# Optimization experiments

Hardware: AMD Instinct MI355X
Metric: run time of the kernel (lower is better)

Reference implementation:

```python
import jax, jax.numpy as jnp
import numpy as np

B, N, DIM = 2, 8192, 3
K = 16            # num_neighbours (dilation=1)
R = 2048          # num_representitives
CIN, CL, COUT = 64, 16, 128
K2 = K * K


def _bn(x, g, b):
    # BatchNorm in eval mode with running_mean=0, running_var=1 -> affine
    return x * g + b


def setup_inputs() -> dict:
    key = jax.random.key(0)
    ks = jax.random.split(key, 24)
    r = lambda i, shape, s=1.0: jax.random.normal(ks[i], shape, jnp.float32) * s
    return {
        "points": r(0, (B, N, DIM)),
        "features": r(1, (B, N, CIN)),
        "lift_w": r(2, (CL, DIM), 0.3), "lift_b": r(3, (CL,), 0.1),
        "bn_lift_g": 1.0 + r(4, (CL,), 0.1), "bn_lift_b": r(5, (CL,), 0.1),
        "t1_w": r(6, (K2, DIM * K), 0.1), "t1_b": r(7, (K2,), 0.1),
        "bn1_g": 1.0 + r(8, (K2,), 0.1), "bn1_b": r(9, (K2,), 0.1),
        "t2_w": r(10, (K2, K2), 0.05), "t2_b": r(11, (K2,), 0.1),
        "bn2_g": 1.0 + r(12, (K2,), 0.1), "bn2_b": r(13, (K2,), 0.1),
        "t3_w": r(14, (K2, K2), 0.05), "t3_b": r(15, (K2,), 0.1),
        "bn3_g": 1.0 + r(16, (K2,), 0.1), "bn3_b": r(17, (K2,), 0.1),
        "conv_w": r(18, (COUT, CIN + CL, K), 0.05), "conv_b": r(19, (COUT,), 0.1),
        "rep_idx": jax.random.permutation(ks[20], N)[:R],
    }


def reference(points, features, lift_w, lift_b, bn_lift_g, bn_lift_b,
              t1_w, t1_b, bn1_g, bn1_b, t2_w, t2_b, bn2_g, bn2_b,
              t3_w, t3_b, bn3_g, bn3_b, conv_w, conv_b, rep_idx):
    b, n, _ = points.shape
    # ---- KNN (squared distance is order-equivalent to torch.cdist) ----
    sq = jnp.sum(points * points, -1)                                   # (b,n)
    d2 = sq[:, :, None] + sq[:, None, :] - 2.0 * jnp.einsum('bnd,bmd->bnm', points, points)
    _, idx = jax.lax.top_k(-d2, K + 1)                                  # (b,n,K+1)
    nn_idx = idx[:, :, 1:]                                              # drop self
    # ---- representative sampling + neighbor gather ----
    rep_pos = points[:, rep_idx]                                        # (b,R,3)
    nb_idx = nn_idx[:, rep_idx]                                         # (b,R,K)
    gather = jax.vmap(lambda arr, i: arr[i])
    nbr_pos = gather(points, nb_idx)                                    # (b,R,K,3)
    nbr_feat = gather(features, nb_idx)                                 # (b,R,K,CIN)
    # ---- X_conv ----
    p = (nbr_pos - rep_pos[:, :, None, :]).reshape(b * R, K, DIM)       # centered
    lifted = jax.nn.relu(_bn(p @ lift_w.T + lift_b, bn_lift_g, bn_lift_b))  # (bR,K,CL)
    feat = jnp.concatenate([lifted, nbr_feat.reshape(b * R, K, CIN)], -1)   # (bR,K,CL+CIN)
    pf = p.reshape(b * R, K * DIM)
    h = jax.nn.relu(_bn(pf @ t1_w.T + t1_b, bn1_g, bn1_b))
    h = jax.nn.relu(_bn(h @ t2_w.T + t2_b, bn2_g, bn2_b))
    T = _bn(h @ t3_w.T + t3_b, bn3_g, bn3_b).reshape(b * R, K, K)       # learned transform
    Tf = jnp.einsum('bij,bjc->bic', T, feat)                            # bmm, (bR,K,C)
    # Conv1d(C, COUT, kernel=K) over length K -> single output position
    out = jnp.einsum('bkc,ock->bo', Tf, conv_w) + conv_b                # (bR,COUT)
    return rep_pos, out.reshape(b, R, COUT)
```

## Files before the change

kernel.cpp:

```cpp
#include <hip/hip_runtime.h>
#include <float.h>

#define Bn 2
#define Nn 8192
#define Rr 2048
#define Kk 16
#define CIN 64
#define CL 16
#define COUT 128
#define K2c 256
#define GT (Bn*Rr)
#define FD (CL+CIN)
#define KC (Kk*FD)
#define MG 8
#define SPLITK 4
#define CCAP 128

__global__ __launch_bounds__(256) void prep_kernel(
    const float* __restrict__ t1_w, const float* __restrict__ t2_w,
    const float* __restrict__ t3_w, const float* __restrict__ conv_w,
    const float* __restrict__ points,
    float* __restrict__ t1t, float* __restrict__ t2t,
    float* __restrict__ t3t, float* __restrict__ wp,
    float4* __restrict__ pts4)
{
  int i = blockIdx.x * 256 + threadIdx.x;
  if (i < K2c*48) { int j = i / 48, k = i - j*48; t1t[k*K2c + j] = t1_w[i]; }
  if (i < K2c*K2c) { int j = i >> 8, k = i & 255; t2t[k*K2c + j] = t2_w[i]; t3t[k*K2c + j] = t3_w[i]; }
  if (i < COUT*KC) {
    int o = i / KC, ck = i - o*KC;
    int c = ck >> 4, k = ck & 15;
    wp[(k*FD + c)*COUT + o] = conv_w[i];
  }
  if (i < Bn*Nn) {
    float x = points[i*3+0], y = points[i*3+1], z = points[i*3+2];
    float sq = __fadd_rn(__fadd_rn(__fmul_rn(x,x), __fmul_rn(y,y)), __fmul_rn(z,z));
    pts4[i] = make_float4(x, y, z, sq);
  }
}

__global__ __launch_bounds__(512, 4) void knn_kernel(
    const float4* __restrict__ pts4, const int* __restrict__ rep_idx,
    int* __restrict__ nb_idx, float* __restrict__ p_out,
    float* __restrict__ rep_pos_out)
{
  __shared__ float cbuf[8][512];
  __shared__ unsigned long long coll[8][CCAP];
  __shared__ float Lst[8][64];
  __shared__ float4 qS[8];
  __shared__ float  tauS[8];
  __shared__ int    ccnt[8];

  int t    = threadIdx.x;
  int lane = t & 63;
  int w    = t >> 6;
  int g0   = blockIdx.x * 8;
  int b    = g0 >> 11;
  const float4* pb4 = pts4 + (size_t)b*Nn;

  if (t < 8) {
    int g = g0 + t;
    int r = g & 2047;
    qS[t] = pb4[rep_idx[r]];
    ccnt[t] = 0;
  }
  __syncthreads();

  float qx[8], qy[8], qz[8], qw[8];
  #pragma unroll
  for (int q = 0; q < 8; q++) {
    float4 Q = qS[q];
    qx[q] = __uint_as_float(__builtin_amdgcn_readfirstlane(__float_as_uint(Q.x)));
    qy[q] = __uint_as_float(__builtin_amdgcn_readfirstlane(__float_as_uint(Q.y)));
    qz[q] = __uint_as_float(__builtin_amdgcn_readfirstlane(__float_as_uint(Q.z)));
    qw[q] = __uint_as_float(__builtin_amdgcn_readfirstlane(__float_as_uint(Q.w)));
  }

  float m[8];
  #pragma unroll
  for (int q = 0; q < 8; q++) m[q] = FLT_MAX;
  for (int i0 = 0; i0 < 16; i0 += 4) {
    float4 P0 = pb4[t + 512*(i0+0)];
    float4 P1 = pb4[t + 512*(i0+1)];
    float4 P2 = pb4[t + 512*(i0+2)];
    float4 P3 = pb4[t + 512*(i0+3)];
    #pragma unroll
    for (int q = 0; q < 8; q++) {
      float d0 = __fsub_rn(__fadd_rn(qw[q], P0.w), __fmul_rn(2.0f,
                 __fmaf_rn(qz[q], P0.z, __fmaf_rn(qy[q], P0.y, __fmul_rn(qx[q], P0.x)))));
      float d1 = __fsub_rn(__fadd_rn(qw[q], P1.w), __fmul_rn(2.0f,
                 __fmaf_rn(qz[q], P1.z, __fmaf_rn(qy[q], P1.y, __fmul_rn(qx[q], P1.x)))));
      float d2 = __fsub_rn(__fadd_rn(qw[q], P2.w), __fmul_rn(2.0f,
                 __fmaf_rn(qz[q], P2.z, __fmaf_rn(qy[q], P2.y, __fmul_rn(qx[q], P2.x)))));
      float d3 = __fsub_rn(__fadd_rn(qw[q], P3.w), __fmul_rn(2.0f,
                 __fmaf_rn(qz[q], P3.z, __fmaf_rn(qy[q], P3.y, __fmul_rn(qx[q], P3.x)))));
      m[q] = fminf(fminf(fminf(m[q], d0), fminf(d1, d2)), d3);
    }
  }

  #pragma unroll
  for (int q = 0; q < 8; q++) cbuf[q][t] = m[q];
  __syncthreads();

  {
    float C0 = FLT_MAX, C1 = FLT_MAX, C2 = FLT_MAX;
    #pragma unroll
    for (int j = 0; j < 8; j++) {
      float v = cbuf[w][lane + 64*j];
      float n2 = __builtin_amdgcn_fmed3f(C1, C2, v);
      float n1 = __builtin_amdgcn_fmed3f(C0, C1, v);
      float n0 = fminf(C0, v);
      C0 = n0; C1 = n1; C2 = n2;
    }
    Lst[w][lane] = C2;
  }
  __syncthreads();
  {
    float L = Lst[w][lane];
    int rk = 0;
    #pragma unroll 8
    for (int i = 0; i < 64; i++) {
      float Li = Lst[w][i];
      rk += (Li < L || (Li == L && i < lane)) ? 1 : 0;
    }
    if (rk == 5) tauS[w] = L;
  }
  __syncthreads();

  float tau[8];
  #pragma unroll
  for (int q = 0; q < 8; q++)
    tau[q] = __uint_as_float(__builtin_amdgcn_readfirstlane(__float_as_uint(tauS[q])));

  for (int i0 = 0; i0 < 16; i0 += 4) {
    float4 Pb[4];
    Pb[0] = pb4[t + 512*(i0+0)];
    Pb[1] = pb4[t + 512*(i0+1)];
    Pb[2] = pb4[t + 512*(i0+2)];
    Pb[3] = pb4[t + 512*(i0+3)];
    #pragma unroll
    for (int u = 0; u < 4; u++) {
      float4 P = Pb[u];
      int idx = t + 512*(i0+u);
      #pragma unroll
      for (int q = 0; q < 8; q++) {
        float dot = __fmaf_rn(qz[q], P.z, __fmaf_rn(qy[q], P.y, __fmul_rn(qx[q], P.x)));
        float d2  = __fsub_rn(__fadd_rn(qw[q], P.w), __fmul_rn(2.0f, dot));
        if (d2 <= tau[q]) {
          int pos = atomicAdd(&ccnt[q], 1);
          if (pos < CCAP) {
            unsigned f = __float_as_uint(d2);
            unsigned mono = f ^ ((unsigned)((int)f >> 31) | 0x80000000u);
            coll[q][pos] = ((unsigned long long)mono << 32) | (unsigned)idx;
          }
        }
      }
    }
  }
  __syncthreads();

  int cnt = __builtin_amdgcn_readfirstlane(ccnt[w]);
  if (cnt > CCAP) cnt = CCAP;
  unsigned long long k1 = (lane < cnt)      ? coll[w][lane]      : ~0ull;
  unsigned long long k2 = (lane + 64 < cnt) ? coll[w][lane + 64] : ~0ull;
  int r1 = 0, r2 = 0;
  for (int i = 0; i < cnt; i++) {
    unsigned long long ki = coll[w][i];
    r1 += (ki < k1) ? 1 : 0;
    r2 += (ki < k2) ? 1 : 0;
  }

  int g = g0 + w;
  float4 Q = qS[w];
  if (lane < cnt && r1 >= 1 && r1 <= 16) {
    int om = (int)(k1 & 0xFFFFFFFFull);
    nb_idx[g*Kk + r1 - 1] = om;
    float4 Pm = pb4[om];
    p_out[(g*Kk + r1 - 1)*3 + 0] = __fsub_rn(Pm.x, Q.x);
    p_out[(g*Kk + r1 - 1)*3 + 1] = __fsub_rn(Pm.y, Q.y);
    p_out[(g*Kk + r1 - 1)*3 + 2] = __fsub_rn(Pm.z, Q.z);
  }
  if (lane + 64 < cnt && r2 >= 1 && r2 <= 16) {
    int om = (int)(k2 & 0xFFFFFFFFull);
    nb_idx[g*Kk + r2 - 1] = om;
    float4 Pm = pb4[om];
    p_out[(g*Kk + r2 - 1)*3 + 0] = __fsub_rn(Pm.x, Q.x);
    p_out[(g*Kk + r2 - 1)*3 + 1] = __fsub_rn(Pm.y, Q.y);
    p_out[(g*Kk + r2 - 1)*3 + 2] = __fsub_rn(Pm.z, Q.z);
  }
  if (lane < 3) rep_pos_out[g*3 + lane] = (lane == 0 ? Q.x : (lane == 1 ? Q.y : Q.z));
}

__device__ __forceinline__ void fma_g(float4& a, float hv, const float4& wv) {
  a.x = fmaf(hv, wv.x, a.x);
  a.y = fmaf(hv, wv.y, a.y);
  a.z = fmaf(hv, wv.z, a.z);
  a.w = fmaf(hv, wv.w, a.w);
}

__global__ __launch_bounds__(256) void mlp_kernel(
    const float* __restrict__ p,
    const float* __restrict__ t1t, const float* __restrict__ t1_b,
    const float* __restrict__ g1v, const float* __restrict__ b1v,
    const float* __restrict__ t2t, const float* __restrict__ t2_b,
    const float* __restrict__ g2v, const float* __restrict__ b2v,
    const float* __restrict__ t3t, const float* __restrict__ t3_b,
    const float* __restrict__ g3v, const float* __restrict__ b3v,
    float* __restrict__ T_out)
{
  __shared__ float pf[48][MG];
  __shared__ float hA[K2c][MG];
  __shared__ float red[4*32*66];
  int t = threadIdx.x;
  int w = t >> 6, l = t & 63;
  int g0 = blockIdx.x * MG;
  for (int e = t; e < MG*48; e += 256) {
    int g = e / 48, k = e - g*48;
    pf[k][g] = p[(size_t)(g0+g)*48 + k];
  }
  __syncthreads();

  float4 acc[MG];

#define LDW(WSRC, K) (*(const float4*)&WSRC[(size_t)(K)*K2c + 4*l])

#define KSTAGE(WSRC, KDIM, HBUF, WB, KK, KNEXT)                        \
  {                                                                    \
    float4 wc = WB;                                                    \
    if ((KNEXT) < KDIM) WB = LDW(WSRC, KNEXT);                         \
    float4 ha = *(const float4*)&HBUF[KK][0];                          \
    float4 hb = *(const float4*)&HBUF[KK][4];                          \
    fma_g(acc[0], ha.x, wc); fma_g(acc[1], ha.y, wc);                  \
    fma_g(acc[2], ha.z, wc); fma_g(acc[3], ha.w, wc);                  \
    fma_g(acc[4], hb.x, wc); fma_g(acc[5], hb.y, wc);                  \
    fma_g(acc[6], hb.z, wc); fma_g(acc[7], hb.w, wc);                  \
  }

#define KLOOP(WSRC, KDIM, HBUF)                                        \
  {                                                                    \
    _Pragma("unroll")                                                  \
    for (int q = 0; q < MG; q++) acc[q] = make_float4(0.f,0.f,0.f,0.f);\
    float4 wb0 = LDW(WSRC, w);                                         \
    float4 wb1 = (w + 4  < KDIM) ? LDW(WSRC, w + 4)  : wb0;            \
    float4 wb2 = (w + 8  < KDIM) ? LDW(WSRC, w + 8)  : wb0;            \
    float4 wb3 = (w + 12 < KDIM) ? LDW(WSRC, w + 12) : wb0;            \
    for (int k = w; k < KDIM; k += 16) {                               \
      KSTAGE(WSRC, KDIM, HBUF, wb0, k,      k + 16)                    \
      if (k + 4 < KDIM)  KSTAGE(WSRC, KDIM, HBUF, wb1, k + 4,  k + 20) \
      if (k + 8 < KDIM)  KSTAGE(WSRC, KDIM, HBUF, wb2, k + 8,  k + 24) \
      if (k + 12 < KDIM) KSTAGE(WSRC, KDIM, HBUF, wb3, k + 12, k + 28) \
    }                                                                  \
  }

#define WRITE_RED()                                                    \
  {                                                                    \
    _Pragma("unroll")                                                  \
    for (int q = 0; q < MG; q++) {                                     \
      red[(w*32 + 0*8 + q)*66 + l] = acc[q].x;                         \
      red[(w*32 + 1*8 + q)*66 + l] = acc[q].y;                         \
      red[(w*32 + 2*8 + q)*66 + l] = acc[q].z;                         \
      red[(w*32 + 3*8 + q)*66 + l] = acc[q].w;                         \
    }                                                                  \
  }

#define REDUCE(S)                                                      \
  float S[MG];                                                         \
  {                                                                    \
    int lr = t >> 2, cc = t & 3;                                       \
    _Pragma("unroll")                                                  \
    for (int q = 0; q < MG; q++) S[q] = 0.f;                           \
    _Pragma("unroll")                                                  \
    for (int ww = 0; ww < 4; ww++) {                                   \
      _Pragma("unroll")                                                \
      for (int q = 0; q < MG; q++)                                     \
        S[q] += red[(ww*32 + cc*8 + q)*66 + lr];                       \
    }                                                                  \
  }

  KLOOP(t1t, 48, pf)
  WRITE_RED()
  __syncthreads();
  {
    REDUCE(s)
    float bb = t1_b[t], gg = g1v[t], oo = b1v[t];
    float4 v0, v1;
    v0.x = fmaxf(fmaf(s[0] + bb, gg, oo), 0.f);
    v0.y = fmaxf(fmaf(s[1] + bb, gg, oo), 0.f);
    v0.z = fmaxf(fmaf(s[2] + bb, gg, oo), 0.f);
    v0.w = fmaxf(fmaf(s[3] + bb, gg, oo), 0.f);
    v1.x = fmaxf(fmaf(s[4] + bb, gg, oo), 0.f);
    v1.y = fmaxf(fmaf(s[5] + bb, gg, oo), 0.f);
    v1.z = fmaxf(fmaf(s[6] + bb, gg, oo), 0.f);
    v1.w = fmaxf(fmaf(s[7] + bb, gg, oo), 0.f);
    *(float4*)&hA[t][0] = v0;
    *(float4*)&hA[t][4] = v1;
  }
  __syncthreads();

  KLOOP(t2t, K2c, hA)
  WRITE_RED()
  __syncthreads();
  {
    REDUCE(s)
    float bb = t2_b[t], gg = g2v[t], oo = b2v[t];
    float4 v0, v1;
    v0.x = fmaxf(fmaf(s[0] + bb, gg, oo), 0.f);
    v0.y = fmaxf(fmaf(s[1] + bb, gg, oo), 0.f);
    v0.z = fmaxf(fmaf(s[2] + bb, gg, oo), 0.f);
    v0.w = fmaxf(fmaf(s[3] + bb, gg, oo), 0.f);
    v1.x = fmaxf(fmaf(s[4] + bb, gg, oo), 0.f);
    v1.y = fmaxf(fmaf(s[5] + bb, gg, oo), 0.f);
    v1.z = fmaxf(fmaf(s[6] + bb, gg, oo), 0.f);
    v1.w = fmaxf(fmaf(s[7] + bb, gg, oo), 0.f);
    *(float4*)&hA[t][0] = v0;
    *(float4*)&hA[t][4] = v1;
  }
  __syncthreads();

  KLOOP(t3t, K2c, hA)
  WRITE_RED()
  __syncthreads();
  {
    REDUCE(s)
    float bb = t3_b[t], gg = g3v[t], oo = b3v[t];
    #pragma unroll
    for (int q = 0; q < MG; q++)
      T_out[(size_t)(g0+q)*K2c + t] = fmaf(s[q] + bb, gg, oo);
  }
#undef KLOOP
#undef KSTAGE
#undef LDW
#undef WRITE_RED
#undef REDUCE
}

__global__ __launch_bounds__(256) void tf_kernel(
    const float* __restrict__ T_in, const float* __restrict__ features,
    const float* __restrict__ p, const int* __restrict__ nb_idx,
    const float* __restrict__ lift_w, const float* __restrict__ lift_b,
    const float* __restrict__ bng, const float* __restrict__ bnb,
    float* __restrict__ Tf)
{
  __shared__ float T_s[4*K2c];
  __shared__ float f_s[4*KC];
  __shared__ float ps[4*48];
  __shared__ int   idxs[64];
  __shared__ float lw[48], lb2[16], lg[16], lo[16];
  int t = threadIdx.x;
  int g0 = blockIdx.x * 4;
  int b = g0 / Rr;
  for (int e = t; e < 4*K2c; e += 256) T_s[e] = T_in[(size_t)g0*K2c + e];
  if (t >= 32 && t < 224) {
    int e = t - 32;
    ps[e] = p[(size_t)g0*48 + e];
  }
  if (t < 64) idxs[t] = nb_idx[g0*16 + t];
  if (t >= 64 && t < 112)  lw[t-64]   = lift_w[t-64];
  if (t >= 112 && t < 128) lb2[t-112] = lift_b[t-112];
  if (t >= 224 && t < 240) lg[t-224]  = bng[t-224];
  if (t >= 240)            lo[t-240]  = bnb[t-240];
  __syncthreads();

  {
    int wv = t >> 6, ln = t & 63;
    for (int row = wv; row < 64; row += 4) {
      int gg = row >> 4, k = row & 15;
      f_s[gg*KC + k*FD + CL + ln] = features[((size_t)b*Nn + idxs[row])*CIN + ln];
    }
  }
  for (int e = t; e < 1024; e += 256) {
    int gg = e >> 8, rem = e & 255, k = rem >> 4, c = rem & 15;
    float acc = ps[gg*48 + k*3 + 0]*lw[c*3+0] + ps[gg*48 + k*3 + 1]*lw[c*3+1]
              + ps[gg*48 + k*3 + 2]*lw[c*3+2] + lb2[c];
    acc = acc*lg[c] + lo[c];
    f_s[gg*KC + k*FD + c] = fmaxf(acc, 0.f);
  }
  __syncthreads();

  int gg = t >> 6;
  int cl = t & 63;
  for (int ci = cl; ci < FD; ci += 64) {
    float fcol[16];
    #pragma unroll
    for (int j = 0; j < 16; j++) fcol[j] = f_s[gg*KC + j*FD + ci];
    #pragma unroll
    for (int k = 0; k < 16; k++) {
      float acc = 0.f;
      #pragma unroll
      for (int j = 0; j < 16; j++) acc = fmaf(T_s[gg*K2c + k*16 + j], fcol[j], acc);
      Tf[(size_t)(g0+gg)*KC + k*FD + ci] = acc;
    }
  }
}

__global__ __launch_bounds__(256) void gemm_kernel(
    const float* __restrict__ A,
    const float* __restrict__ Bm,
    float* __restrict__ part)
{
  __shared__ float As[16*36];
  __shared__ float Bs[16*COUT];
  int t = threadIdx.x;
  int m0 = blockIdx.x * 32;
  int ky = blockIdx.y;
  int kbase0 = ky * (KC/SPLITK);
  float acc[4][4];
  #pragma unroll
  for (int i = 0; i < 4; i++)
    #pragma unroll
    for (int j = 0; j < 4; j++) acc[i][j] = 0.f;
  int tn = t & 31, tm = t >> 5;

  for (int kt = 0; kt < KC/SPLITK; kt += 16) {
    int kb = kbase0 + kt;
    {
      int kcol = t & 15, row = t >> 4;
      As[kcol*36 + row]      = A[(size_t)(m0+row)*KC + kb + kcol];
      As[kcol*36 + row + 16] = A[(size_t)(m0+row+16)*KC + kb + kcol];
    }
    {
      int o = t & 127, kk2 = t >> 7;
      #pragma unroll
      for (int p4 = 0; p4 < 8; p4++) {
        int kk = kk2 + p4*2;
        Bs[kk*COUT + o] = Bm[(size_t)(kb+kk)*COUT + o];
      }
    }
    __syncthreads();
    #pragma unroll
    for (int kk = 0; kk < 16; kk++) {
      float4 a4 = *(const float4*)&As[kk*36 + tm*4];
      float4 b4 = *(const float4*)&Bs[kk*COUT + tn*4];
      float av[4] = {a4.x, a4.y, a4.z, a4.w};
      float bv[4] = {b4.x, b4.y, b4.z, b4.w};
      #pragma unroll
      for (int i = 0; i < 4; i++)
        #pragma unroll
        for (int j = 0; j < 4; j++) acc[i][j] = fmaf(av[i], bv[j], acc[i][j]);
    }
    __syncthreads();
  }
  #pragma unroll
  for (int i = 0; i < 4; i++) {
    float4 v = make_float4(acc[i][0], acc[i][1], acc[i][2], acc[i][3]);
    *(float4*)&part[((size_t)ky*GT + m0 + tm*4 + i)*COUT + tn*4] = v;
  }
}

__global__ __launch_bounds__(256) void reduce_kernel(
    const float* __restrict__ part, const float* __restrict__ conv_b,
    float* __restrict__ outp)
{
  int i = blockIdx.x*256 + threadIdx.x;
  float4 s = ((const float4*)conv_b)[i & 31];
  #pragma unroll
  for (int w = 0; w < SPLITK; w++) {
    float4 v = ((const float4*)(part + (size_t)w*GT*COUT))[i];
    s.x += v.x; s.y += v.y; s.z += v.z; s.w += v.w;
  }
  ((float4*)outp)[i] = s;
}

extern "C" void kernel_launch(void* const* d_in, const int* in_sizes, int n_in,
                              void* d_out, int out_size, void* d_ws, size_t ws_size,
                              hipStream_t stream) {
  const float* points   = (const float*)d_in[0];
  const float* features = (const float*)d_in[1];
  const float* lift_w   = (const float*)d_in[2];
  const float* lift_b   = (const float*)d_in[3];
  const float* bn_lift_g= (const float*)d_in[4];
  const float* bn_lift_b= (const float*)d_in[5];
  const float* t1_w     = (const float*)d_in[6];
  const float* t1_b     = (const float*)d_in[7];
  const float* bn1_g    = (const float*)d_in[8];
  const float* bn1_b    = (const float*)d_in[9];
  const float* t2_w     = (const float*)d_in[10];
  const float* t2_b     = (const float*)d_in[11];
  const float* bn2_g    = (const float*)d_in[12];
  const float* bn2_b    = (const float*)d_in[13];
  const float* t3_w     = (const float*)d_in[14];
  const float* t3_b     = (const float*)d_in[15];
  const float* bn3_g    = (const float*)d_in[16];
  const float* bn3_b    = (const float*)d_in[17];
  const float* conv_w   = (const float*)d_in[18];
  const float* conv_b   = (const float*)d_in[19];
  const int*   rep_idx  = (const int*)d_in[20];

  char* ws = (char*)d_ws;
  int*    nb   = (int*)   (ws + 0);
  float*  p    = (float*) (ws + 262144);
  float*  T    = (float*) (ws + 1048576);
  float*  Tf   = (float*) (ws + 5242880);
  float*  wp   = (float*) (ws + 26214400);
  float*  t1t  = (float*) (ws + 26869760);
  float*  t2t  = (float*) (ws + 26918912);
  float*  t3t  = (float*) (ws + 27181056);
  float*  part = (float*) (ws + 33554432);
  float4* pts4 = (float4*)(ws + 52428800);

  float* rep_pos = (float*)d_out;
  float* outp    = (float*)d_out + (size_t)GT*3;

  prep_kernel<<<640, 256, 0, stream>>>(t1_w, t2_w, t3_w, conv_w, points,
                                       t1t, t2t, t3t, wp, pts4);
  knn_kernel<<<GT/8, 512, 0, stream>>>(pts4, rep_idx, nb, p, rep_pos);
  mlp_kernel<<<GT/MG, 256, 0, stream>>>(p, t1t, t1_b, bn1_g, bn1_b,
                                        t2t, t2_b, bn2_g, bn2_b,
                                        t3t, t3_b, bn3_g, bn3_b, T);
  tf_kernel<<<GT/4, 256, 0, stream>>>(T, features, p, nb,
                                      lift_w, lift_b, bn_lift_g, bn_lift_b, Tf);
  dim3 ggrid(GT/32, SPLITK);
  gemm_kernel<<<ggrid, 256, 0, stream>>>(Tf, wp, part);
  reduce_kernel<<<(GT*COUT/4)/256, 256, 0, stream>>>(part, conv_b, outp);
}
```

Measured before the change: 216.2 us.

## Double MLP kernel block to 512 threads with split-K across eight wavefronts

```diff
diff --git a/kernel.cpp b/kernel.cpp
--- a/kernel.cpp
+++ b/kernel.cpp
@@ -12,7 +12,7 @@
 #define GT (Bn*Rr)
 #define FD (CL+CIN)
 #define KC (Kk*FD)
-#define MG 8
+#define MGB 8
 #define SPLITK 4
 #define CCAP 128
 
@@ -198,7 +198,7 @@
   a.w = fmaf(hv, wv.w, a.w);
 }
 
-__global__ __launch_bounds__(256) void mlp_kernel(
+__global__ __launch_bounds__(512) void mlp_kernel(
     const float* __restrict__ p,
     const float* __restrict__ t1t, const float* __restrict__ t1_b,
     const float* __restrict__ g1v, const float* __restrict__ b1v,
@@ -208,19 +208,22 @@
     const float* __restrict__ g3v, const float* __restrict__ b3v,
     float* __restrict__ T_out)
 {
-  __shared__ float pf[48][MG];
-  __shared__ float hA[K2c][MG];
-  __shared__ float red[4*32*66];
+  __shared__ float pf[48][MGB];
+  __shared__ float hA[K2c][MGB];
+  __shared__ float red[128*66];
   int t = threadIdx.x;
   int w = t >> 6, l = t & 63;
-  int g0 = blockIdx.x * MG;
-  for (int e = t; e < MG*48; e += 256) {
+  int g0 = blockIdx.x * MGB;
+  for (int e = t; e < MGB*48; e += 512) {
     int g = e / 48, k = e - g*48;
     pf[k][g] = p[(size_t)(g0+g)*48 + k];
   }
   __syncthreads();
 
-  float4 acc[MG];
+  float4 acc[MGB];
+  int col = t & 255;
+  int h   = t >> 8;
+  int cc  = col & 3, lr = col >> 2;
 
 #define LDW(WSRC, K) (*(const float4*)&WSRC[(size_t)(K)*K2c + 4*l])
 
@@ -239,93 +242,91 @@
 #define KLOOP(WSRC, KDIM, HBUF)                                        \
   {                                                                    \
     _Pragma("unroll")                                                  \
-    for (int q = 0; q < MG; q++) acc[q] = make_float4(0.f,0.f,0.f,0.f);\
+    for (int q = 0; q < MGB; q++) acc[q] = make_float4(0.f,0.f,0.f,0.f);\
     float4 wb0 = LDW(WSRC, w);                                         \
-    float4 wb1 = (w + 4  < KDIM) ? LDW(WSRC, w + 4)  : wb0;            \
-    float4 wb2 = (w + 8  < KDIM) ? LDW(WSRC, w + 8)  : wb0;            \
-    float4 wb3 = (w + 12 < KDIM) ? LDW(WSRC, w + 12) : wb0;            \
-    for (int k = w; k < KDIM; k += 16) {                               \
-      KSTAGE(WSRC, KDIM, HBUF, wb0, k,      k + 16)                    \
-      if (k + 4 < KDIM)  KSTAGE(WSRC, KDIM, HBUF, wb1, k + 4,  k + 20) \
-      if (k + 8 < KDIM)  KSTAGE(WSRC, KDIM, HBUF, wb2, k + 8,  k + 24) \
-      if (k + 12 < KDIM) KSTAGE(WSRC, KDIM, HBUF, wb3, k + 12, k + 28) \
+    float4 wb1 = (w + 8  < KDIM) ? LDW(WSRC, w + 8)  : wb0;            \
+    float4 wb2 = (w + 16 < KDIM) ? LDW(WSRC, w + 16) : wb0;            \
+    float4 wb3 = (w + 24 < KDIM) ? LDW(WSRC, w + 24) : wb0;            \
+    for (int k = w; k < KDIM; k += 32) {                               \
+      KSTAGE(WSRC, KDIM, HBUF, wb0, k,      k + 32)                    \
+      if (k + 8  < KDIM) KSTAGE(WSRC, KDIM, HBUF, wb1, k + 8,  k + 40) \
+      if (k + 16 < KDIM) KSTAGE(WSRC, KDIM, HBUF, wb2, k + 16, k + 48) \
+      if (k + 24 < KDIM) KSTAGE(WSRC, KDIM, HBUF, wb3, k + 24, k + 56) \
     }                                                                  \
   }
 
 #define WRITE_RED()                                                    \
   {                                                                    \
-    _Pragma("unroll")                                                  \
-    for (int q = 0; q < MG; q++) {                                     \
-      red[(w*32 + 0*8 + q)*66 + l] = acc[q].x;                         \
-      red[(w*32 + 1*8 + q)*66 + l] = acc[q].y;                         \
-      red[(w*32 + 2*8 + q)*66 + l] = acc[q].z;                         \
-      red[(w*32 + 3*8 + q)*66 + l] = acc[q].w;                         \
+    if (w < 4) {                                                       \
+      _Pragma("unroll")                                                \
+      for (int q = 0; q < MGB; q++) {                                  \
+        red[((w*4 + 0)*8 + q)*66 + l] = acc[q].x;                      \
+        red[((w*4 + 1)*8 + q)*66 + l] = acc[q].y;                      \
+        red[((w*4 + 2)*8 + q)*66 + l] = acc[q].z;                      \
+        red[((w*4 + 3)*8 + q)*66 + l] = acc[q].w;                      \
+      }                                                                \
     }                                                                  \
+    __syncthreads();                                                   \
+    if (w >= 4) {                                                      \
+      int w2 = w - 4;                                                  \
+      _Pragma("unroll")                                                \
+      for (int q = 0; q < MGB; q++) {                                  \
+        red[((w2*4 + 0)*8 + q)*66 + l] += acc[q].x;                    \
+        red[((w2*4 + 1)*8 + q)*66 + l] += acc[q].y;                    \
+        red[((w2*4 + 2)*8 + q)*66 + l] += acc[q].z;                    \
+        red[((w2*4 + 3)*8 + q)*66 + l] += acc[q].w;                    \
+      }                                                                \
+    }                                                                  \
+    __syncthreads();                                                   \
   }
 
 #define REDUCE(S)                                                      \
-  float S[MG];                                                         \
+  float S[4] = {0.f, 0.f, 0.f, 0.f};                                   \
   {                                                                    \
-    int lr = t >> 2, cc = t & 3;                                       \
-    _Pragma("unroll")                                                  \
-    for (int q = 0; q < MG; q++) S[q] = 0.f;                           \
     _Pragma("unroll")                                                  \
     for (int ww = 0; ww < 4; ww++) {                                   \
       _Pragma("unroll")                                                \
-      for (int q = 0; q < MG; q++)                                     \
-        S[q] += red[(ww*32 + cc*8 + q)*66 + lr];                       \
+      for (int qi = 0; qi < 4; qi++)                                   \
+        S[qi] += red[((ww*4 + cc)*8 + (h*4 + qi))*66 + lr];            \
     }                                                                  \
   }
 
   KLOOP(t1t, 48, pf)
   WRITE_RED()
-  __syncthreads();
   {
     REDUCE(s)
-    float bb = t1_b[t], gg = g1v[t], oo = b1v[t];
-    float4 v0, v1;
-    v0.x = fmaxf(fmaf(s[0] + bb, gg, oo), 0.f);
-    v0.y = fmaxf(fmaf(s[1] + bb, gg, oo), 0.f);
-    v0.z = fmaxf(fmaf(s[2] + bb, gg, oo), 0.f);
-    v0.w = fmaxf(fmaf(s[3] + bb, gg, oo), 0.f);
-    v1.x = fmaxf(fmaf(s[4] + bb, gg, oo), 0.f);
-    v1.y = fmaxf(fmaf(s[5] + bb, gg, oo), 0.f);
-    v1.z = fmaxf(fmaf(s[6] + bb, gg, oo), 0.f);
-    v1.w = fmaxf(fmaf(s[7] + bb, gg, oo), 0.f);
-    *(float4*)&hA[t][0] = v0;
-    *(float4*)&hA[t][4] = v1;
+    float bb = t1_b[col], gg = g1v[col], oo = b1v[col];
+    float4 v;
+    v.x = fmaxf(fmaf(s[0] + bb, gg, oo), 0.f);
+    v.y = fmaxf(fmaf(s[1] + bb, gg, oo), 0.f);
+    v.z = fmaxf(fmaf(s[2] + bb, gg, oo), 0.f);
+    v.w = fmaxf(fmaf(s[3] + bb, gg, oo), 0.f);
+    *(float4*)&hA[col][h*4] = v;
   }
   __syncthreads();
 
   KLOOP(t2t, K2c, hA)
   WRITE_RED()
-  __syncthreads();
   {
     REDUCE(s)
-    float bb = t2_b[t], gg = g2v[t], oo = b2v[t];
-    float4 v0, v1;
-    v0.x = fmaxf(fmaf(s[0] + bb, gg, oo), 0.f);
-    v0.y = fmaxf(fmaf(s[1] + bb, gg, oo), 0.f);
-    v0.z = fmaxf(fmaf(s[2] + bb, gg, oo), 0.f);
-    v0.w = fmaxf(fmaf(s[3] + bb, gg, oo), 0.f);
-    v1.x = fmaxf(fmaf(s[4] + bb, gg, oo), 0.f);
-    v1.y = fmaxf(fmaf(s[5] + bb, gg, oo), 0.f);
-    v1.z = fmaxf(fmaf(s[6] + bb, gg, oo), 0.f);
-    v1.w = fmaxf(fmaf(s[7] + bb, gg, oo), 0.f);
-    *(float4*)&hA[t][0] = v0;
-    *(float4*)&hA[t][4] = v1;
+    float bb = t2_b[col], gg = g2v[col], oo = b2v[col];
+    float4 v;
+    v.x = fmaxf(fmaf(s[0] + bb, gg, oo), 0.f);
+    v.y = fmaxf(fmaf(s[1] + bb, gg, oo), 0.f);
+    v.z = fmaxf(fmaf(s[2] + bb, gg, oo), 0.f);
+    v.w = fmaxf(fmaf(s[3] + bb, gg, oo), 0.f);
+    *(float4*)&hA[col][h*4] = v;
   }
   __syncthreads();
 
   KLOOP(t3t, K2c, hA)
   WRITE_RED()
-  __syncthreads();
   {
     REDUCE(s)
-    float bb = t3_b[t], gg = g3v[t], oo = b3v[t];
-    #pragma unroll
-    for (int q = 0; q < MG; q++)
-      T_out[(size_t)(g0+q)*K2c + t] = fmaf(s[q] + bb, gg, oo);
+    float bb = t3_b[col], gg = g3v[col], oo = b3v[col];
+    #pragma unroll
+    for (int qi = 0; qi < 4; qi++)
+      T_out[(size_t)(g0 + h*4 + qi)*K2c + col] = fmaf(s[qi] + bb, gg, oo);
   }
 #undef KLOOP
 #undef KSTAGE
@@ -504,9 +505,9 @@
   prep_kernel<<<640, 256, 0, stream>>>(t1_w, t2_w, t3_w, conv_w, points,
                                        t1t, t2t, t3t, wp, pts4);
   knn_kernel<<<GT/8, 512, 0, stream>>>(pts4, rep_idx, nb, p, rep_pos);
-  mlp_kernel<<<GT/MG, 256, 0, stream>>>(p, t1t, t1_b, bn1_g, bn1_b,
-                                        t2t, t2_b, bn2_g, bn2_b,
-                                        t3t, t3_b, bn3_g, bn3_b, T);
+  mlp_kernel<<<GT/MGB, 512, 0, stream>>>(p, t1t, t1_b, bn1_g, bn1_b,
+                                         t2t, t2_b, bn2_g, bn2_b,
+                                         t3t, t3_b, bn3_g, bn3_b, T);
   tf_kernel<<<GT/4, 256, 0, stream>>>(T, features, p, nb,
                                       lift_w, lift_b, bn_lift_g, bn_lift_b, Tf);
   dim3 ggrid(GT/32, SPLITK);
```

New measurement: 201.6 us. -6.7%, faster.
